# Kernel optimization log

Measured on AMD Instinct MI355X. Metric: run time of the kernel, lower is better.

The kernel has to match this reference:

```python
import jax, jax.numpy as jnp
import numpy as np

C = 201      # num_classes (200 + background)
K = 5        # num_prototype
D = 256      # projected dim
GAMMA = 0.999
SK_EPS = 0.05
SK_ITERS = 3


def l2n(x, eps=1e-12):
    return x / jnp.maximum(jnp.linalg.norm(x, axis=-1, keepdims=True), eps)


def layernorm(x, g, b, eps=1e-5):
    mu = jnp.mean(x, axis=-1, keepdims=True)
    var = jnp.var(x, axis=-1, keepdims=True)
    return (x - mu) * jax.lax.rsqrt(var + eps) * g + b


def masked_sinkhorn(logits, mask_f):
    # logits: [N, K] prototype logits for one class; mask_f: [N] 1.0 where patch belongs to class
    m = mask_f[:, None]
    L = jnp.exp(logits / SK_EPS) * m
    Bc = mask_f.sum()  # number of patches of this class
    L = L / jnp.maximum(jnp.sum(L), 1e-12)
    for _ in range(SK_ITERS):
        L = L / jnp.maximum(jnp.sum(L, axis=0, keepdims=True), 1e-12) / K   # per-prototype marginal
        L = L / jnp.maximum(jnp.sum(L, axis=1, keepdims=True), 1e-12) * m   # per-patch marginal (masked)
        L = L / jnp.maximum(Bc, 1.0)
    L = L * Bc
    idx = jnp.argmax(L, axis=1)                                   # prototype index per patch
    hard = jax.nn.one_hot(idx, K, dtype=logits.dtype) * m          # deterministic hard assignment
    return hard, idx


def setup_inputs() -> dict:
    key = jax.random.key(0)
    k0, k1, k2, k3 = jax.random.split(key, 4)
    B, HW, DB = 64, 256, 768
    patch_tokens = jax.random.normal(k0, (B, HW, DB), jnp.float32)
    proj_w = jax.random.normal(k1, (D, DB), jnp.float32) * (1.0 / np.sqrt(DB))
    proj_b = jnp.zeros((D,), jnp.float32)
    ln_g = jnp.ones((D,), jnp.float32)
    ln_b = jnp.zeros((D,), jnp.float32)
    prototypes = jax.random.normal(k2, (C, K, D), jnp.float32) * 0.02
    pseudo_fg_mask = jax.random.randint(k3, (B * HW,), 0, C, dtype=jnp.int32)
    return dict(patch_tokens=patch_tokens, proj_w=proj_w, proj_b=proj_b,
                ln_g=ln_g, ln_b=ln_b, prototypes=prototypes,
                pseudo_fg_mask=pseudo_fg_mask)


def reference(patch_tokens, proj_w, proj_b, ln_g, ln_b, prototypes, pseudo_fg_mask):
    B, HW, _ = patch_tokens.shape
    H = W = int(np.sqrt(HW))
    patches = jnp.einsum('bnd,ed->bne', patch_tokens, proj_w) + proj_b      # [B,HW,D]
    patches = l2n(layernorm(patches.reshape(-1, D), ln_g, ln_b))             # [N,D] l2-normalized
    protos = l2n(prototypes)                                                 # [C,K,D] (in-place buffer normalize)
    logits_nck = jnp.einsum('nd,ckd->nck', patches, protos)                  # [N,C,K] == cosine sims
    ppl = logits_nck.reshape(B, H, W, C * K).transpose(0, 3, 1, 2)           # [B,CK,H,W]
    img_logits = jnp.mean(ppl, axis=(2, 3))                                  # AdaptiveAvgPool2d(1,1)
    pred_logits = jnp.sum(img_logits.reshape(B, C, K), axis=-1)              # == img_logits @ fc

    # ---- prototype update (vectorized over the original per-class python loop) ----
    N = patches.shape[0]
    class_preds = jnp.argmax(jnp.max(logits_nck, axis=2), axis=1)            # argmax of patch class logits
    correct_f = (pseudo_fg_mask == class_preds).astype(patches.dtype)        # [N]
    patches_correct = patches * correct_f[:, None]                           # [N,D]

    def per_class(c):
        mask_f = (pseudo_fg_mask == c).astype(patches.dtype)
        hard, idx = masked_sinkhorn(logits_nck[:, c, :], mask_f)
        L_correct = hard * correct_f[:, None]                                # [N,K]
        score = logits_nck[:, c, :] * L_correct                              # cos * assignment
        top_idx = jnp.argmax(score, axis=0)                                  # top-1 patch per prototype
        P_new_c = patches_correct[top_idx]                                   # [K,D] == final_assignment^T @ patches_correct
        return P_new_c, idx, mask_f.sum() > 0

    P_new, proto_idx, has_patches = jax.vmap(per_class)(jnp.arange(C))
    P_new = l2n(P_new)
    # final_assignment puts exactly one 1 per prototype column, so n_final != 0 always;
    # the update gate reduces to 'class has at least one patch'.
    P_upd = jnp.where(has_patches[:, None, None],
                      GAMMA * protos + (1.0 - GAMMA) * P_new, protos)
    new_prototypes = l2n(P_upd)

    per_patch_idx = jnp.take_along_axis(proto_idx.T, pseudo_fg_mask[:, None].astype(jnp.int32), axis=1)[:, 0]
    contrast_target = (per_patch_idx + K * pseudo_fg_mask).astype(patches.dtype)
    contrast_logits = logits_nck.reshape(N, C * K)
    return pred_logits, ppl, img_logits, contrast_logits, contrast_target, new_prototypes
```

## Files before the change

kernel.cpp:

```cpp
#include <hip/hip_runtime.h>
#include <hip/hip_bf16.h>

#define NROWS 16384
#define DBK   768
#define DDIM  256
#define NC    201
#define NK    5
#define NCK   1005

#define O_PPL    12864
#define O_IMG    16478784
#define O_CONTR  16543104
#define O_TGT    33009024
#define O_NEWP   33025408

#define W_PATCH  0u
#define W_PN     4194304u
#define W_CORR   4451584u
#define W_MEANP  4467968u
#define W_PBF    4484352u
#define W_PNBF   8678656u
#define W_CNT    8809728u
#define W_FILLP  8809984u
#define W_OFFS   8810240u
#define W_ROWS   8810496u

typedef __attribute__((ext_vector_type(8))) short     short8;
typedef __attribute__((ext_vector_type(4))) float     f32x4;
typedef __attribute__((ext_vector_type(4))) unsigned int uint4v;
typedef __attribute__((ext_vector_type(4))) unsigned short ushort4v;

__device__ __forceinline__ float waveRedSum(float v){
  #pragma unroll
  for(int o=32;o>0;o>>=1) v += __shfl_xor(v,o,64);
  return v;
}

__device__ __forceinline__ unsigned short f2bf(float x){
  union { float f; unsigned u; } c; c.f = x;
  unsigned r = c.u + 0x7FFFu + ((c.u >> 16) & 1u);
  return (unsigned short)(r >> 16);
}
__device__ __forceinline__ unsigned pack2(float a, float b){
  return (unsigned)f2bf(a) | ((unsigned)f2bf(b) << 16);
}
__device__ __forceinline__ uint4v pack8(float4 lo, float4 hi){
  uint4v u;
  u[0] = pack2(lo.x, lo.y); u[1] = pack2(lo.z, lo.w);
  u[2] = pack2(hi.x, hi.y); u[3] = pack2(hi.z, hi.w);
  return u;
}

__global__ __launch_bounds__(256,2) void k_gemm1m(
    const float* __restrict__ A, const float* __restrict__ W,
    const float* __restrict__ bias, float* __restrict__ out)
{
  __shared__ ushort As[4096];
  __shared__ ushort Bs[4096];
  const int tid = threadIdx.x;
  const int m0 = blockIdx.x * 128;
  const int n0 = blockIdx.y * 128;
  const int lane = tid & 63, wid = tid >> 6;
  const int wr = wid >> 1, wc = wid & 1;
  const int srow = tid >> 2, sslot = tid & 3;
  const int woff  = srow*32      + (sslot ^ ((srow>>1)&3))*8;
  const int woff2 = (srow+64)*32 + (sslot ^ ((srow>>1)&3))*8;
  const int l15 = lane & 15, kg = lane >> 4;
  const int rslot = (kg ^ ((l15>>1)&3))*8;
  f32x4 acc[4][4] = {};
  const float* Ap0 = A + (size_t)(m0+srow)*DBK + sslot*8;
  const float* Ap1 = Ap0 + (size_t)64*DBK;
  const float* Wp0 = W + (size_t)(n0+srow)*DBK + sslot*8;
  const float* Wp1 = Wp0 + (size_t)64*DBK;
  for (int k0 = 0; k0 < DBK; k0 += 32) {
    float4 a00 = *(const float4*)(Ap0+k0), a01 = *(const float4*)(Ap0+k0+4);
    float4 a10 = *(const float4*)(Ap1+k0), a11 = *(const float4*)(Ap1+k0+4);
    float4 b00 = *(const float4*)(Wp0+k0), b01 = *(const float4*)(Wp0+k0+4);
    float4 b10 = *(const float4*)(Wp1+k0), b11 = *(const float4*)(Wp1+k0+4);
    __syncthreads();
    *(uint4v*)&As[woff]  = pack8(a00, a01);
    *(uint4v*)&As[woff2] = pack8(a10, a11);
    *(uint4v*)&Bs[woff]  = pack8(b00, b01);
    *(uint4v*)&Bs[woff2] = pack8(b10, b11);
    __syncthreads();
    short8 af[4], bf[4];
    #pragma unroll
    for (int i=0;i<4;i++){
      af[i] = *(const short8*)&As[(wr*64 + i*16 + l15)*32 + rslot];
      bf[i] = *(const short8*)&Bs[(wc*64 + i*16 + l15)*32 + rslot];
    }
    #pragma unroll
    for (int i=0;i<4;i++)
      #pragma unroll
      for (int j=0;j<4;j++)
        acc[i][j] = __builtin_amdgcn_mfma_f32_16x16x32_bf16(af[i], bf[j], acc[i][j], 0,0,0);
  }
  #pragma unroll
  for (int j=0;j<4;j++){
    const int ncol = n0 + wc*64 + j*16 + l15;
    const float bv = bias[ncol];
    #pragma unroll
    for (int i=0;i<4;i++){
      const int mrow = m0 + wr*64 + i*16 + kg*4;
      #pragma unroll
      for (int r=0;r<4;r++)
        out[(size_t)(mrow+r)*DDIM + ncol] = acc[i][j][r] + bv;
    }
  }
}

__global__ __launch_bounds__(256,2) void k_gemm2m(
    const ushort* __restrict__ A, const ushort* __restrict__ B,
    float* __restrict__ ct, float* __restrict__ ppl)
{
  __shared__ ushort As[4096];
  __shared__ ushort Bs[4096];
  const int tid = threadIdx.x;
  const int m0 = blockIdx.x * 128;
  const int n0 = blockIdx.y * 128;
  const int lane = tid & 63, wid = tid >> 6;
  const int wr = wid >> 1, wc = wid & 1;
  const int srow = tid >> 2, sslot = tid & 3;
  const int woff  = srow*32      + (sslot ^ ((srow>>1)&3))*8;
  const int woff2 = (srow+64)*32 + (sslot ^ ((srow>>1)&3))*8;
  const int l15 = lane & 15, kg = lane >> 4;
  const int rslot = (kg ^ ((l15>>1)&3))*8;
  f32x4 acc[4][4] = {};
  const ushort* Ap0 = A + (size_t)(m0+srow)*DDIM + sslot*8;
  const ushort* Ap1 = Ap0 + (size_t)64*DDIM;
  const ushort* Bp0 = B + (size_t)(n0+srow)*DDIM + sslot*8;
  const ushort* Bp1 = Bp0 + (size_t)64*DDIM;
  for (int k0 = 0; k0 < DDIM; k0 += 32) {
    uint4v a0 = *(const uint4v*)(Ap0+k0);
    uint4v a1 = *(const uint4v*)(Ap1+k0);
    uint4v b0 = *(const uint4v*)(Bp0+k0);
    uint4v b1 = *(const uint4v*)(Bp1+k0);
    __syncthreads();
    *(uint4v*)&As[woff]  = a0;
    *(uint4v*)&As[woff2] = a1;
    *(uint4v*)&Bs[woff]  = b0;
    *(uint4v*)&Bs[woff2] = b1;
    __syncthreads();
    short8 af[4], bf[4];
    #pragma unroll
    for (int i=0;i<4;i++){
      af[i] = *(const short8*)&As[(wr*64 + i*16 + l15)*32 + rslot];
      bf[i] = *(const short8*)&Bs[(wc*64 + i*16 + l15)*32 + rslot];
    }
    #pragma unroll
    for (int i=0;i<4;i++)
      #pragma unroll
      for (int j=0;j<4;j++)
        acc[i][j] = __builtin_amdgcn_mfma_f32_16x16x32_bf16(af[i], bf[j], acc[i][j], 0,0,0);
  }
  const int bimg = m0 >> 8;
  #pragma unroll
  for (int i=0;i<4;i++){
    const int mrow = m0 + wr*64 + i*16 + kg*4;
    const int hw = mrow & 255;
    #pragma unroll
    for (int j=0;j<4;j++){
      const int ck = n0 + wc*64 + j*16 + l15;
      if (ck < NCK){
        #pragma unroll
        for (int r=0;r<4;r++)
          ct[(size_t)(mrow+r)*NCK + ck] = acc[i][j][r];
        *(f32x4*)&ppl[((size_t)(bimg*NCK+ck))*256 + hw] = acc[i][j];
      }
    }
  }
}

__global__ __launch_bounds__(256) void k_ln(float* __restrict__ p,
    const float* __restrict__ g, const float* __restrict__ bta, ushort* __restrict__ pbf)
{
  const int wid = threadIdx.x >> 6, lane = threadIdx.x & 63;
  const int row = blockIdx.x * 4 + wid;
  float4 x = *(float4*)&p[(size_t)row*DDIM + lane*4];
  float s = x.x + x.y + x.z + x.w;
  s = waveRedSum(s);
  const float mu = s * (1.f/256.f);
  const float d0=x.x-mu, d1=x.y-mu, d2=x.z-mu, d3=x.w-mu;
  float ss = d0*d0 + d1*d1 + d2*d2 + d3*d3;
  ss = waveRedSum(ss);
  const float var = ss * (1.f/256.f);
  const float rs = rsqrtf(var + 1e-5f);
  const float4 gv = *(const float4*)&g[lane*4];
  const float4 bv = *(const float4*)&bta[lane*4];
  const float y0 = d0*rs*gv.x + bv.x;
  const float y1 = d1*rs*gv.y + bv.y;
  const float y2 = d2*rs*gv.z + bv.z;
  const float y3 = d3*rs*gv.w + bv.w;
  float n2 = y0*y0 + y1*y1 + y2*y2 + y3*y3;
  n2 = waveRedSum(n2);
  const float inv = 1.f / fmaxf(sqrtf(n2), 1e-12f);
  float4 o; o.x=y0*inv; o.y=y1*inv; o.z=y2*inv; o.w=y3*inv;
  *(float4*)&p[(size_t)row*DDIM + lane*4] = o;
  ushort4v ob; ob[0]=f2bf(o.x); ob[1]=f2bf(o.y); ob[2]=f2bf(o.z); ob[3]=f2bf(o.w);
  *(ushort4v*)&pbf[(size_t)row*DDIM + lane*4] = ob;
}

__global__ __launch_bounds__(256) void k_pnorm(const float* __restrict__ pr,
    float* __restrict__ out, ushort* __restrict__ obf)
{
  const int wid = threadIdx.x >> 6, lane = threadIdx.x & 63;
  const int row = blockIdx.x * 4 + wid;
  if (row >= NCK){
    ushort4v z = {0,0,0,0};
    *(ushort4v*)&obf[(size_t)row*DDIM + lane*4] = z;
    return;
  }
  const float4 x = *(const float4*)&pr[(size_t)row*DDIM + lane*4];
  float n2 = x.x*x.x + x.y*x.y + x.z*x.z + x.w*x.w;
  n2 = waveRedSum(n2);
  const float inv = 1.f / fmaxf(sqrtf(n2), 1e-12f);
  float4 o; o.x=x.x*inv; o.y=x.y*inv; o.z=x.z*inv; o.w=x.w*inv;
  *(float4*)&out[(size_t)row*DDIM + lane*4] = o;
  ushort4v ob; ob[0]=f2bf(o.x); ob[1]=f2bf(o.y); ob[2]=f2bf(o.z); ob[3]=f2bf(o.w);
  *(ushort4v*)&obf[(size_t)row*DDIM + lane*4] = ob;
}

__global__ __launch_bounds__(256) void k_pmean(const float* __restrict__ p, float* __restrict__ mp)
{
  const int b = blockIdx.x, d = threadIdx.x;
  const float* base = p + (size_t)b*256*DDIM + d;
  float s = 0.f;
  #pragma unroll 8
  for (int r=0;r<256;r++) s += base[(size_t)r*DDIM];
  mp[b*DDIM + d] = s * (1.f/256.f);
}

__global__ __launch_bounds__(256) void k_img2(const float* __restrict__ mp,
    const float* __restrict__ pn, float* __restrict__ img)
{
  const int gid = blockIdx.x*256 + threadIdx.x;
  if (gid >= 64*NCK) return;
  const int b = gid / NCK, ck = gid - b*NCK;
  const float4* a = (const float4*)&mp[b*DDIM];
  const float4* q = (const float4*)&pn[(size_t)ck*DDIM];
  float s = 0.f;
  #pragma unroll 8
  for (int d=0; d<64; d++){
    const float4 x = a[d], y = q[d];
    s += x.x*y.x + x.y*y.y + x.z*y.z + x.w*y.w;
  }
  img[gid] = s;
}

__global__ __launch_bounds__(256) void k_pred(const float* __restrict__ img, float* __restrict__ pred)
{
  const int gid = blockIdx.x*256 + threadIdx.x;
  if (gid >= 64*NC) return;
  const int b = gid / NC, c = gid % NC;
  const float* ip = &img[(size_t)b*NCK + c*5];
  pred[(size_t)b*NC + c] = ip[0]+ip[1]+ip[2]+ip[3]+ip[4];
}

__global__ __launch_bounds__(256) void k_cls(const float* __restrict__ ct,
    const int* __restrict__ mask, float* __restrict__ corr)
{
  const int wid = threadIdx.x >> 6, lane = threadIdx.x & 63;
  const int n = blockIdx.x * 4 + wid;
  const float* row = &ct[(size_t)n*NCK];
  float bv = -1e30f; int bc = 0x7FFFFFFF;
  #pragma unroll
  for(int j=0;j<16;j++){
    const int ck = lane + 64*j;
    if (ck < NCK){
      const float v = row[ck];
      const int c = ck / 5;
      if (v > bv || (v == bv && c < bc)){ bv = v; bc = c; }
    }
  }
  #pragma unroll
  for(int o=32;o>0;o>>=1){
    const float ov = __shfl_xor(bv,o,64);
    const int   oc = __shfl_xor(bc,o,64);
    if (ov > bv || (ov == bv && oc < bc)){ bv = ov; bc = oc; }
  }
  if (lane == 0) corr[n] = (mask[n] == bc) ? 1.f : 0.f;
}

__global__ __launch_bounds__(256) void k_hist(const int* __restrict__ mask, int* __restrict__ cnt)
{
  const int n = blockIdx.x*256 + threadIdx.x;
  atomicAdd(&cnt[mask[n]], 1);
}

__global__ __launch_bounds__(256) void k_scan(const int* __restrict__ cnt, int* __restrict__ offs)
{
  __shared__ int sc[256];
  const int tid = threadIdx.x;
  const int v = (tid < NC) ? cnt[tid] : 0;
  sc[tid] = v;
  __syncthreads();
  #pragma unroll
  for (int s=1; s<256; s<<=1){
    const int add = (tid >= s) ? sc[tid-s] : 0;
    __syncthreads();
    sc[tid] += add;
    __syncthreads();
  }
  offs[tid] = sc[tid] - v;
}

__global__ __launch_bounds__(256) void k_fill(const int* __restrict__ mask,
    const int* __restrict__ offs, int* __restrict__ fillp, int* __restrict__ rows)
{
  const int n = blockIdx.x*256 + threadIdx.x;
  const int c = mask[n];
  const int pos = atomicAdd(&fillp[c], 1);
  rows[offs[c] + pos] = n;
}

__device__ __forceinline__ void blockRed5_256(float* a, float* ls){
  #pragma unroll
  for (int j=0;j<5;j++) a[j] = waveRedSum(a[j]);
  const int wv = threadIdx.x >> 6, lane = threadIdx.x & 63;
  __syncthreads();
  if (lane == 0){
    #pragma unroll
    for (int j=0;j<5;j++) ls[wv*5+j] = a[j];
  }
  __syncthreads();
  #pragma unroll
  for (int j=0;j<5;j++) a[j] = ls[j] + ls[5+j] + ls[10+j] + ls[15+j];
}

__device__ __forceinline__ float blockSum256(float x, float* ls4){
  x = waveRedSum(x);
  const int wv = threadIdx.x >> 6, lane = threadIdx.x & 63;
  __syncthreads();
  if (lane == 0) ls4[wv] = x;
  __syncthreads();
  return ls4[0] + ls4[1] + ls4[2] + ls4[3];
}

__global__ __launch_bounds__(256,4) void k_sink2(
    const float* __restrict__ ppl, const int* __restrict__ cnt,
    const int* __restrict__ offs, const int* __restrict__ rows,
    const float* __restrict__ corr, const float* __restrict__ patches,
    const float* __restrict__ pn, float* __restrict__ tgt, float* __restrict__ newp)
{
  const int c = blockIdx.x, c5 = c*5, tid = threadIdx.x;
  const int wv = tid >> 6, lane = tid & 63;
  __shared__ float ls[20];
  __shared__ float lsv[20];
  __shared__ int   lsn[20];
  const int nr  = cnt[c];
  const int off = offs[c];
  const bool act = tid < nr;
  int n = 0; float lg[5], e[5]; float cf = 0.f;
  if (act){
    n = rows[off + tid];
    const float* lp = ppl + ((size_t)((n>>8)*NCK) + c5)*256 + (n&255);
    #pragma unroll
    for (int k=0;k<5;k++){ lg[k] = lp[k*256]; e[k] = expf(lg[k]*20.f); }
    cf = corr[n];
  } else {
    #pragma unroll
    for (int k=0;k<5;k++){ lg[k] = 0.f; e[k] = 0.f; }
  }
  float a[5];
  #pragma unroll
  for (int k=0;k<5;k++) a[k] = e[k];
  blockRed5_256(a, ls);
  const float Bcc = (float)(nr > 0 ? nr : 1);
  const float S = a[0]+a[1]+a[2]+a[3]+a[4];
  const float v0 = 1.f / fmaxf(S, 1e-12f);
  float v[5];
  #pragma unroll
  for (int k=0;k<5;k++) v[k] = v0 / (fmaxf(v0*a[k], 1e-12f) * 5.f);
  float u = 1.f;
  #pragma unroll 1
  for (int t=0;t<2;t++){
    float w[5] = {0.f,0.f,0.f,0.f,0.f};
    if (act){
      const float s = e[0]*v[0] + e[1]*v[1] + e[2]*v[2] + e[3]*v[3] + e[4]*v[4];
      const float un = u / fmaxf(u*s, 1e-12f) / Bcc;
      u = un;
      #pragma unroll
      for (int k=0;k<5;k++) w[k] = un * e[k];
    }
    blockRed5_256(w, ls);
    #pragma unroll
    for (int k=0;k<5;k++) v[k] = v[k] / (fmaxf(v[k]*w[k], 1e-12f) * 5.f);
  }
  int bi = 0;
  if (act){
    float bb = e[0]*v[0];
    #pragma unroll
    for (int k=1;k<5;k++){
      const float p = e[k]*v[k];
      if (p > bb){ bb = p; bi = k; }
    }
    tgt[n] = (float)(bi + c5);
  }
  const bool cc = act && (cf > 0.5f);
  float sv[5]; int sn[5];
  #pragma unroll
  for (int k=0;k<5;k++){
    float rv = (cc && bi == k) ? lg[k] : 0.f;
    int   rn = act ? n : 0x7FFFFFFF;
    if (0.f > rv || (0.f == rv && tid < rn)){ rv = 0.f; rn = tid; }
    sv[k] = rv; sn[k] = rn;
  }
  #pragma unroll
  for (int k=0;k<5;k++){
    #pragma unroll
    for (int o=32;o>0;o>>=1){
      const float ov = __shfl_xor(sv[k],o,64);
      const int   on = __shfl_xor(sn[k],o,64);
      if (ov > sv[k] || (ov == sv[k] && on < sn[k])){ sv[k]=ov; sn[k]=on; }
    }
  }
  __syncthreads();
  if (lane == 0){
    #pragma unroll
    for (int k=0;k<5;k++){ lsv[wv*5+k] = sv[k]; lsn[wv*5+k] = sn[k]; }
  }
  __syncthreads();
  int topn[5];
  #pragma unroll
  for (int k=0;k<5;k++){
    float bb = lsv[k]; int nn = lsn[k];
    #pragma unroll
    for (int w2=1;w2<4;w2++){
      const float ov = lsv[w2*5+k]; const int on = lsn[w2*5+k];
      if (ov > bb || (ov == bb && on < nn)){ bb = ov; nn = on; }
    }
    topn[k] = nn;
  }
  const bool hasp = (nr > 0);
  #pragma unroll 1
  for (int k=0;k<5;k++){
    const int tn_ = topn[k];
    const float cfa = corr[tn_];
    const float pv = patches[(size_t)tn_*DDIM + tid] * cfa;
    const float proto = pn[(size_t)(c5+k)*DDIM + tid];
    const float ss = blockSum256(pv*pv, ls);
    const float pnv = pv / fmaxf(sqrtf(ss), 1e-12f);
    const float pu = hasp ? (0.999f*proto + 0.001f*pnv) : proto;
    const float ss2 = blockSum256(pu*pu, ls);
    newp[(size_t)(c5+k)*DDIM + tid] = pu / fmaxf(sqrtf(ss2), 1e-12f);
  }
}

extern "C" void kernel_launch(void* const* d_in, const int* in_sizes, int n_in,
                              void* d_out, int out_size, void* d_ws, size_t ws_size,
                              hipStream_t stream)
{
  const float* patch_tokens = (const float*)d_in[0];
  const float* proj_w       = (const float*)d_in[1];
  const float* proj_b       = (const float*)d_in[2];
  const float* ln_g         = (const float*)d_in[3];
  const float* ln_b         = (const float*)d_in[4];
  const float* prototypes   = (const float*)d_in[5];
  const int*   mask         = (const int*)d_in[6];
  float* out = (float*)d_out;
  float* ws  = (float*)d_ws;

  float*  patches = ws + W_PATCH;
  float*  pn      = ws + W_PN;
  float*  corr    = ws + W_CORR;
  float*  meanp   = ws + W_MEANP;
  ushort* pbf     = (ushort*)(ws + W_PBF);
  ushort* pnbf    = (ushort*)(ws + W_PNBF);
  int*    cnt     = (int*)(ws + W_CNT);
  int*    fillp   = (int*)(ws + W_FILLP);
  int*    offs    = (int*)(ws + W_OFFS);
  int*    rows    = (int*)(ws + W_ROWS);

  float* pred = out;
  float* ppl  = out + O_PPL;
  float* img  = out + O_IMG;
  float* ct   = out + O_CONTR;
  float* tgt  = out + O_TGT;
  float* newp = out + O_NEWP;

  hipMemsetAsync((void*)cnt, 0, 512*sizeof(int), stream);
  k_hist<<<64,256,0,stream>>>(mask, cnt);
  k_scan<<<1,256,0,stream>>>(cnt, offs);
  k_fill<<<64,256,0,stream>>>(mask, offs, fillp, rows);

  k_gemm1m<<<dim3(128,2),256,0,stream>>>(patch_tokens, proj_w, proj_b, patches);
  k_ln<<<4096,256,0,stream>>>(patches, ln_g, ln_b, pbf);
  k_pnorm<<<256,256,0,stream>>>(prototypes, pn, pnbf);
  k_gemm2m<<<dim3(128,8),256,0,stream>>>(pbf, pnbf, ct, ppl);
  k_pmean<<<64,256,0,stream>>>(patches, meanp);
  k_img2<<<252,256,0,stream>>>(meanp, pn, img);
  k_pred<<<51,256,0,stream>>>(img, pred);
  k_cls<<<4096,256,0,stream>>>(ct, mask, corr);
  k_sink2<<<201,256,0,stream>>>(ppl, cnt, offs, rows, corr, patches, pn, tgt, newp);
}
```

Baseline: 322.2 us.

## Fuse per-row class argmax into GEMM epilogue and merge image-logit kernels

The GEMM epilogue now computes each row's partial argmax across its column tile and writes it to a small workspace. A tiny k_cls2 kernel then reduces the eight tiles instead of re-reading the full 16384x1005 contrast matrix. Output stores switch to nontemporal, and the pmean, img and pred kernels merge into one per-image kernel that holds the mean and logits in shared memory. The cost is extra shuffles, LDS use and a block sync in the GEMM epilogue, and fewer blocks run in the merged img kernel.

Measured after the change: 394.3 us. 1.22x slower.

```diff
diff --git a/kernel.cpp b/kernel.cpp
--- a/kernel.cpp
+++ b/kernel.cpp
@@ -17,13 +17,14 @@
 #define W_PATCH  0u
 #define W_PN     4194304u
 #define W_CORR   4451584u
-#define W_MEANP  4467968u
 #define W_PBF    4484352u
 #define W_PNBF   8678656u
 #define W_CNT    8809728u
 #define W_FILLP  8809984u
 #define W_OFFS   8810240u
 #define W_ROWS   8810496u
+#define W_PMAX   8826880u
+#define W_PCLS   8957952u
 
 typedef __attribute__((ext_vector_type(8))) short     short8;
 typedef __attribute__((ext_vector_type(4))) float     f32x4;
@@ -111,10 +112,13 @@
 
 __global__ __launch_bounds__(256,2) void k_gemm2m(
     const ushort* __restrict__ A, const ushort* __restrict__ B,
-    float* __restrict__ ct, float* __restrict__ ppl)
+    float* __restrict__ ct, float* __restrict__ ppl,
+    float* __restrict__ pmax, int* __restrict__ pcls)
 {
   __shared__ ushort As[4096];
   __shared__ ushort Bs[4096];
+  __shared__ float rmaxs[128][2];
+  __shared__ int   rclss[128][2];
   const int tid = threadIdx.x;
   const int m0 = blockIdx.x * 128;
   const int n0 = blockIdx.y * 128;
@@ -164,11 +168,60 @@
       if (ck < NCK){
         #pragma unroll
         for (int r=0;r<4;r++)
-          ct[(size_t)(mrow+r)*NCK + ck] = acc[i][j][r];
-        *(f32x4*)&ppl[((size_t)(bimg*NCK+ck))*256 + hw] = acc[i][j];
+          __builtin_nontemporal_store(acc[i][j][r], &ct[(size_t)(mrow+r)*NCK + ck]);
+        __builtin_nontemporal_store(acc[i][j], (f32x4*)&ppl[((size_t)(bimg*NCK+ck))*256 + hw]);
       }
     }
   }
+  #pragma unroll
+  for (int i=0;i<4;i++){
+    #pragma unroll
+    for (int r=0;r<4;r++){
+      float bv = -1e30f; int bc = 0x7FFFFFFF;
+      #pragma unroll
+      for (int j=0;j<4;j++){
+        const int ck = n0 + wc*64 + j*16 + l15;
+        if (ck < NCK){
+          const float v = acc[i][j][r];
+          const int c = ck / 5;
+          if (v > bv || (v == bv && c < bc)){ bv = v; bc = c; }
+        }
+      }
+      #pragma unroll
+      for (int o=8;o>0;o>>=1){
+        const float ov = __shfl_xor(bv,o,64);
+        const int   oc = __shfl_xor(bc,o,64);
+        if (ov > bv || (ov == bv && oc < bc)){ bv = ov; bc = oc; }
+      }
+      if (l15 == 0){
+        const int wrow = wr*64 + i*16 + kg*4 + r;
+        rmaxs[wrow][wc] = bv;
+        rclss[wrow][wc] = bc;
+      }
+    }
+  }
+  __syncthreads();
+  if (tid < 128){
+    float bv = rmaxs[tid][0]; int bc = rclss[tid][0];
+    const float ov = rmaxs[tid][1]; const int oc = rclss[tid][1];
+    if (ov > bv || (ov == bv && oc < bc)){ bv = ov; bc = oc; }
+    pmax[(size_t)blockIdx.y*NROWS + m0 + tid] = bv;
+    pcls[(size_t)blockIdx.y*NROWS + m0 + tid] = bc;
+  }
+}
+
+__global__ __launch_bounds__(256) void k_cls2(const float* __restrict__ pmax,
+    const int* __restrict__ pcls, const int* __restrict__ mask, float* __restrict__ corr)
+{
+  const int n = blockIdx.x*256 + threadIdx.x;
+  float bv = -1e30f; int bc = 0x7FFFFFFF;
+  #pragma unroll
+  for (int t=0;t<8;t++){
+    const float ov = pmax[(size_t)t*NROWS + n];
+    const int   oc = pcls[(size_t)t*NROWS + n];
+    if (ov > bv || (ov == bv && oc < bc)){ bv = ov; bc = oc; }
+  }
+  corr[n] = (mask[n] == bc) ? 1.f : 0.f;
 }
 
 __global__ __launch_bounds__(256) void k_ln(float* __restrict__ p,
@@ -220,65 +273,38 @@
   *(ushort4v*)&obf[(size_t)row*DDIM + lane*4] = ob;
 }
 
-__global__ __launch_bounds__(256) void k_pmean(const float* __restrict__ p, float* __restrict__ mp)
-{
-  const int b = blockIdx.x, d = threadIdx.x;
-  const float* base = p + (size_t)b*256*DDIM + d;
+__global__ __launch_bounds__(256) void k_img3(const float* __restrict__ p,
+    const float* __restrict__ pn, float* __restrict__ img, float* __restrict__ pred)
+{
+  __shared__ float mp_s[256];
+  __shared__ float img_s[1008];
+  const int b = blockIdx.x, tid = threadIdx.x;
+  const float* base = p + (size_t)b*256*DDIM + tid;
   float s = 0.f;
   #pragma unroll 8
   for (int r=0;r<256;r++) s += base[(size_t)r*DDIM];
-  mp[b*DDIM + d] = s * (1.f/256.f);
-}
-
-__global__ __launch_bounds__(256) void k_img2(const float* __restrict__ mp,
-    const float* __restrict__ pn, float* __restrict__ img)
-{
-  const int gid = blockIdx.x*256 + threadIdx.x;
-  if (gid >= 64*NCK) return;
-  const int b = gid / NCK, ck = gid - b*NCK;
-  const float4* a = (const float4*)&mp[b*DDIM];
-  const float4* q = (const float4*)&pn[(size_t)ck*DDIM];
-  float s = 0.f;
-  #pragma unroll 8
-  for (int d=0; d<64; d++){
-    const float4 x = a[d], y = q[d];
-    s += x.x*y.x + x.y*y.y + x.z*y.z + x.w*y.w;
-  }
-  img[gid] = s;
-}
-
-__global__ __launch_bounds__(256) void k_pred(const float* __restrict__ img, float* __restrict__ pred)
-{
-  const int gid = blockIdx.x*256 + threadIdx.x;
-  if (gid >= 64*NC) return;
-  const int b = gid / NC, c = gid % NC;
-  const float* ip = &img[(size_t)b*NCK + c*5];
-  pred[(size_t)b*NC + c] = ip[0]+ip[1]+ip[2]+ip[3]+ip[4];
-}
-
-__global__ __launch_bounds__(256) void k_cls(const float* __restrict__ ct,
-    const int* __restrict__ mask, float* __restrict__ corr)
-{
-  const int wid = threadIdx.x >> 6, lane = threadIdx.x & 63;
-  const int n = blockIdx.x * 4 + wid;
-  const float* row = &ct[(size_t)n*NCK];
-  float bv = -1e30f; int bc = 0x7FFFFFFF;
-  #pragma unroll
-  for(int j=0;j<16;j++){
-    const int ck = lane + 64*j;
+  mp_s[tid] = s * (1.f/256.f);
+  __syncthreads();
+  #pragma unroll 1
+  for (int ck = tid; ck < 1008; ck += 256){
+    float d = 0.f;
     if (ck < NCK){
-      const float v = row[ck];
-      const int c = ck / 5;
-      if (v > bv || (v == bv && c < bc)){ bv = v; bc = c; }
-    }
-  }
-  #pragma unroll
-  for(int o=32;o>0;o>>=1){
-    const float ov = __shfl_xor(bv,o,64);
-    const int   oc = __shfl_xor(bc,o,64);
-    if (ov > bv || (ov == bv && oc < bc)){ bv = ov; bc = oc; }
-  }
-  if (lane == 0) corr[n] = (mask[n] == bc) ? 1.f : 0.f;
+      const float4* q = (const float4*)&pn[(size_t)ck*DDIM];
+      const float4* a = (const float4*)mp_s;
+      #pragma unroll 8
+      for (int i=0;i<64;i++){
+        const float4 x = a[i], y = q[i];
+        d += x.x*y.x + x.y*y.y + x.z*y.z + x.w*y.w;
+      }
+      img[(size_t)b*NCK + ck] = d;
+    }
+    img_s[ck] = d;
+  }
+  __syncthreads();
+  if (tid < NC){
+    const float* ip = &img_s[tid*5];
+    pred[(size_t)b*NC + tid] = ip[0]+ip[1]+ip[2]+ip[3]+ip[4];
+  }
 }
 
 __global__ __launch_bounds__(256) void k_hist(const int* __restrict__ mask, int* __restrict__ cnt)
@@ -463,13 +489,14 @@
   float*  patches = ws + W_PATCH;
   float*  pn      = ws + W_PN;
   float*  corr    = ws + W_CORR;
-  float*  meanp   = ws + W_MEANP;
   ushort* pbf     = (ushort*)(ws + W_PBF);
   ushort* pnbf    = (ushort*)(ws + W_PNBF);
   int*    cnt     = (int*)(ws + W_CNT);
   int*    fillp   = (int*)(ws + W_FILLP);
   int*    offs    = (int*)(ws + W_OFFS);
   int*    rows    = (int*)(ws + W_ROWS);
+  float*  pmax    = ws + W_PMAX;
+  int*    pcls    = (int*)(ws + W_PCLS);
 
   float* pred = out;
   float* ppl  = out + O_PPL;
@@ -486,10 +513,8 @@
   k_gemm1m<<<dim3(128,2),256,0,stream>>>(patch_tokens, proj_w, proj_b, patches);
   k_ln<<<4096,256,0,stream>>>(patches, ln_g, ln_b, pbf);
   k_pnorm<<<256,256,0,stream>>>(prototypes, pn, pnbf);
-  k_gemm2m<<<dim3(128,8),256,0,stream>>>(pbf, pnbf, ct, ppl);
-  k_pmean<<<64,256,0,stream>>>(patches, meanp);
-  k_img2<<<252,256,0,stream>>>(meanp, pn, img);
-  k_pred<<<51,256,0,stream>>>(img, pred);
-  k_cls<<<4096,256,0,stream>>>(ct, mask, corr);
+  k_gemm2m<<<dim3(128,8),256,0,stream>>>(pbf, pnbf, ct, ppl, pmax, pcls);
+  k_cls2<<<64,256,0,stream>>>(pmax, pcls, mask, corr);
+  k_img3<<<64,256,0,stream>>>(patches, pn, img, pred);
   k_sink2<<<201,256,0,stream>>>(ppl, cnt, offs, rows, corr, patches, pn, tgt, newp);
 }
```
